# Kernel optimization log

Measured on AMD Instinct MI355X. Metric: run time of the kernel, lower is better.

The kernel has to match this reference:

```python
import jax, jax.numpy as jnp
import numpy as np

N_NODES = 100000
N_EDGES = 1600000
FEATS = 128
HIDDEN = 64
N_CLASS = 40
NEG_SLOPE = 0.01  # torch leaky_relu default


def _glorot(key, shape):
    lim = float(np.sqrt(6.0 / (shape[0] + shape[1])))
    return jax.random.uniform(key, shape, jnp.float32, -lim, lim)


def setup_inputs() -> dict:
    key = jax.random.key(0)
    ks = jax.random.split(key, 10)
    x = jax.random.normal(ks[0], (N_NODES, FEATS), jnp.float32)
    edge_index = jax.random.randint(ks[1], (2, N_EDGES), 0, N_NODES, jnp.int64)
    edge_weight = jax.random.uniform(ks[2], (N_EDGES,), jnp.float32)
    return {
        "x": x,
        "edge_index": edge_index,
        "edge_weight": edge_weight,
        "W_first": _glorot(ks[3], (FEATS, HIDDEN)),
        "b_first": jnp.zeros((HIDDEN,), jnp.float32),
        "Wc1": _glorot(ks[4], (HIDDEN, HIDDEN)),
        "bc1": jnp.zeros((HIDDEN,), jnp.float32),
        "Wc2": _glorot(ks[5], (HIDDEN, HIDDEN)),
        "bc2": jnp.zeros((HIDDEN,), jnp.float32),
        "W_out": _glorot(ks[6], (HIDDEN, N_CLASS)),
        "b_out": jnp.zeros((N_CLASS,), jnp.float32),
    }


def _gcn_norm(edge_index, edge_weight, n):
    # PyG gcn_norm with add_self_loops=True: A_hat = D^-1/2 (A + I) D^-1/2
    loop = jnp.arange(n, dtype=edge_index.dtype)
    src = jnp.concatenate([edge_index[0], loop])
    dst = jnp.concatenate([edge_index[1], loop])
    ew = jnp.concatenate([edge_weight, jnp.ones((n,), edge_weight.dtype)])
    deg = jax.ops.segment_sum(ew, dst, num_segments=n)  # degree at target
    dis = jnp.where(deg > 0, jax.lax.rsqrt(deg), 0.0)
    norm = dis[src] * ew * dis[dst]  # [E+N]
    return src, dst, norm


def _gcn_conv(h, src, dst, norm, W, b, n):
    h = h @ W                                   # [N, H]
    msg = norm[:, None] * h[src]                # gather + scale  [E+N, H]
    out = jax.ops.segment_sum(msg, dst, num_segments=n)  # scatter-add
    return out + b


def reference(x, edge_index, edge_weight, W_first, b_first, Wc1, bc1, Wc2, bc2, W_out, b_out):
    n = x.shape[0]
    src, dst, norm = _gcn_norm(edge_index, edge_weight, n)
    h = jax.nn.leaky_relu(x @ W_first + b_first, NEG_SLOPE)
    # dropout is identity in eval mode
    h = jax.nn.leaky_relu(_gcn_conv(h, src, dst, norm, Wc1, bc1, n), NEG_SLOPE)
    h = jax.nn.leaky_relu(_gcn_conv(h, src, dst, norm, Wc2, bc2, n), NEG_SLOPE)
    logits = h @ W_out + b_out
    return jax.nn.log_softmax(logits, axis=-1)
```

## Files before the change

### kernel.cpp

```cpp
#include <hip/hip_runtime.h>
#include <hip/hip_bf16.h>
#include <math.h>

#define NFEATS 128
#define NHID   64
#define NCLS   40
#define NEG_SLOPE 0.01f

#define GSH_S  9
#define GSPAN_S 512
#define GCAP_S 9216
#define SB     2048

typedef float f32x4 __attribute__((ext_vector_type(4)));
typedef int   i32x2 __attribute__((ext_vector_type(2)));

__device__ inline unsigned short f2bfu(float v) {
    union { float f; unsigned int u; } x; x.f = v;
    unsigned int r = (x.u + 0x7FFFu + ((x.u >> 16) & 1u)) >> 16;
    return (unsigned short)r;
}
__device__ inline float bf2f(unsigned short u) {
    union { unsigned int u32; float f; } x; x.u32 = ((unsigned int)u) << 16;
    return x.f;
}

__device__ inline void role_split(int i, int nA, int nB, int* ia, int* ib) {
    *ia = -1; *ib = -1;
    int m2 = 2 * min(nA, nB);
    if (i < m2) { if (i & 1) *ib = i >> 1; else *ia = i >> 1; }
    else if (nA > nB) *ia = i - nB;
    else *ib = i - nA;
}


__global__ __launch_bounds__(256) void stage_gemm1_kernel(
    const int* __restrict__ srcA, const int* __restrict__ dstA, const float* __restrict__ ew,
    int* __restrict__ gcur, int2* __restrict__ staged, int E, int nStage, int ngrp,
    const float* __restrict__ x, const float* __restrict__ W1, const float* __restrict__ b1,
    float* __restrict__ h1, int n, int nTile) {
    __shared__ __align__(16) float Ws[64 * 64];

    int ia, ib;
    role_split(blockIdx.x, nStage, nTile, &ia, &ib);
    int tid = threadIdx.x;

    if (ia >= 0) {
        int* hist = (int*)Ws;
        int* wcur = ((int*)Ws) + 256;
        if (tid < 256) hist[tid] = 0;
        __syncthreads();

        int q0 = (ia * SB) >> 2;
        int qend = min(q0 + SB / 4, E >> 2);
        int dcache[8], scache[8];
        float wcache[8];

#pragma unroll
        for (int it = 0; it < 2; ++it) {
            int q = q0 + it * 256 + tid;
            bool ok = (q < qend);
            int4 d4 = ok ? ((const int4*)dstA)[q] : make_int4(-1, -1, -1, -1);
            int4 s4 = ok ? ((const int4*)srcA)[q] : make_int4(0, 0, 0, 0);
            float4 w4 = ok ? ((const float4*)ew)[q] : make_float4(0, 0, 0, 0);
            dcache[it * 4 + 0] = d4.x; dcache[it * 4 + 1] = d4.y;
            dcache[it * 4 + 2] = d4.z; dcache[it * 4 + 3] = d4.w;
            scache[it * 4 + 0] = s4.x; scache[it * 4 + 1] = s4.y;
            scache[it * 4 + 2] = s4.z; scache[it * 4 + 3] = s4.w;
            wcache[it * 4 + 0] = w4.x; wcache[it * 4 + 1] = w4.y;
            wcache[it * 4 + 2] = w4.z; wcache[it * 4 + 3] = w4.w;
#pragma unroll
            for (int j = 0; j < 4; ++j)
                if (dcache[it * 4 + j] >= 0) atomicAdd(&hist[dcache[it * 4 + j] >> GSH_S], 1);
        }
        if (ia == nStage - 1) {
            for (int e = (E & ~3) + tid; e < E; e += 256) atomicAdd(&hist[dstA[e] >> GSH_S], 1);
        }
        __syncthreads();

        if (tid < ngrp) {
            int c = hist[tid];
            wcur[tid] = (c > 0) ? atomicAdd(&gcur[tid], c) : 0;
        }
        __syncthreads();

        int pos[8];
#pragma unroll
        for (int j = 0; j < 8; ++j) {
            int d = dcache[j];
            pos[j] = (d >= 0) ? atomicAdd(&wcur[d >> GSH_S], 1) : GCAP_S;
        }
#pragma unroll
        for (int j = 0; j < 8; ++j) {
            int d = dcache[j];
            if (d >= 0 && pos[j] < GCAP_S)
                staged[(size_t)(d >> GSH_S) * GCAP_S + pos[j]] =
                    make_int2(((d & (GSPAN_S - 1)) << 17) | scache[j], __float_as_int(wcache[j]));
        }
        if (ia == nStage - 1) {
            for (int e = (E & ~3) + tid; e < E; e += 256) {
                int d = dstA[e];
                int g = d >> GSH_S;
                int p = atomicAdd(&wcur[g], 1);
                if (p < GCAP_S)
                    staged[(size_t)g * GCAP_S + p] =
                        make_int2(((d & (GSPAN_S - 1)) << 17) | srcA[e], __float_as_int(ew[e]));
            }
        }
        return;
    }

    int c4 = (tid & 15) * 4;
    int r0 = ib * 64 + (tid >> 4) * 4;
    int rr[4];
#pragma unroll
    for (int i = 0; i < 4; ++i) rr[i] = min(r0 + i, n - 1);

    float acc[4][4] = {};
    for (int ph = 0; ph < 2; ++ph) {
        __syncthreads();
        for (int i = tid; i < 64 * 16; i += 256)
            ((float4*)Ws)[i] = ((const float4*)W1)[ph * 1024 + i];
        __syncthreads();
#pragma unroll 2
        for (int kk = 0; kk < 64; kk += 4) {
            f32x4 av[4], bv[4];
#pragma unroll
            for (int i = 0; i < 4; ++i)
                av[i] = __builtin_nontemporal_load(
                    (const f32x4*)&x[(size_t)rr[i] * NFEATS + ph * 64 + kk]);
#pragma unroll
            for (int q = 0; q < 4; ++q) bv[q] = *(const f32x4*)&Ws[(kk + q) * 64 + c4];
#pragma unroll
            for (int i = 0; i < 4; ++i) {
#pragma unroll
                for (int q = 0; q < 4; ++q) {
                    float a = av[i][q];
#pragma unroll
                    for (int j = 0; j < 4; ++j) acc[i][j] += a * bv[q][j];
                }
            }
        }
    }

#pragma unroll
    for (int i = 0; i < 4; ++i) {
        int rw = r0 + i;
        if (rw >= n) break;
        float4 o;
        float* oa = (float*)&o;
#pragma unroll
        for (int j = 0; j < 4; ++j) {
            float v = acc[i][j] + b1[c4 + j];
            oa[j] = (v > 0.0f) ? v : v * NEG_SLOPE;
        }
        *(float4*)&h1[(size_t)rw * 64 + c4] = o;
    }
}


__global__ __launch_bounds__(512) void degsort_kernel(
    const int* __restrict__ gcur, const int2* __restrict__ staged,
    int2* __restrict__ staged2, float* __restrict__ dis,
    int2* __restrict__ nodeptr, int n) {
    __shared__ float deg[GSPAN_S];
    __shared__ int hist[GSPAN_S], base[GSPAN_S], cur[GSPAN_S];

    int tid = threadIdx.x;
    int g = blockIdx.x;
    deg[tid] = 0.0f;
    hist[tid] = 0;
    __syncthreads();

    int cnt = min(gcur[g], GCAP_S);
    const int2* sl = staged + (size_t)g * GCAP_S;
    for (int i = tid; i < cnt; i += 512) {
        int2 r = sl[i];
        int dl = r.x >> 17;
        atomicAdd(&deg[dl], __int_as_float(r.y));
        atomicAdd(&hist[dl], 1);
    }
    __syncthreads();

    int node = g * GSPAN_S + tid;
    if (node < n) dis[node] = rsqrtf(1.0f + deg[tid]);

    base[tid] = hist[tid];
    __syncthreads();
    for (int off = 1; off < GSPAN_S; off <<= 1) {
        int t_ = (tid >= off) ? base[tid - off] : 0;
        __syncthreads();
        base[tid] += t_;
        __syncthreads();
    }
    int ex = base[tid] - hist[tid];
    base[tid] = ex;
    cur[tid] = ex;
    __syncthreads();

    if (node < n) nodeptr[node] = make_int2(g * GCAP_S + ex, hist[tid]);

    int2* out = staged2 + (size_t)g * GCAP_S;
    for (int i = tid; i < cnt; i += 512) {
        int2 r = sl[i];
        int dl = r.x >> 17;
        int pos = atomicAdd(&cur[dl], 1);
        out[pos] = make_int2(r.x & 0x1FFFF, r.y);
    }
}


__global__ __launch_bounds__(256) void gemm2s_kernel(
    const float* __restrict__ in, const float* __restrict__ W, const float* __restrict__ dis,
    unsigned short* __restrict__ outp, int n) {
    __shared__ __align__(16) float Ws[NHID * 64];
    int tid = threadIdx.x;
    for (int i = tid; i < NHID * 16; i += 256) ((float4*)Ws)[i] = ((const float4*)W)[i];
    __syncthreads();

    int c4 = (tid & 15) * 4;
    int r0 = blockIdx.x * 64 + (tid >> 4) * 4;
    int rr[4];
#pragma unroll
    for (int i = 0; i < 4; ++i) rr[i] = min(r0 + i, n - 1);

    float acc[4][4] = {};
#pragma unroll 2
    for (int kk = 0; kk < NHID; kk += 4) {
        f32x4 av[4], bv[4];
#pragma unroll
        for (int i = 0; i < 4; ++i)
            av[i] = __builtin_nontemporal_load((const f32x4*)&in[(size_t)rr[i] * NHID + kk]);
#pragma unroll
        for (int q = 0; q < 4; ++q) bv[q] = *(const f32x4*)&Ws[(kk + q) * 64 + c4];
#pragma unroll
        for (int i = 0; i < 4; ++i) {
#pragma unroll
            for (int q = 0; q < 4; ++q) {
                float a = av[i][q];
#pragma unroll
                for (int j = 0; j < 4; ++j) acc[i][j] += a * bv[q][j];
            }
        }
    }

#pragma unroll
    for (int i = 0; i < 4; ++i) {
        int rw = r0 + i;
        if (rw >= n) break;
        float dr = dis[rw];
        ushort4 o;
        o.x = f2bfu(dr * acc[i][0]); o.y = f2bfu(dr * acc[i][1]);
        o.z = f2bfu(dr * acc[i][2]); o.w = f2bfu(dr * acc[i][3]);
        *(ushort4*)&outp[(size_t)rw * 64 + c4] = o;
    }
}


template <int LAYER>
__global__ __launch_bounds__(256) void agg_kernel(const int2* __restrict__ nodeptr,
                                                  const int2* __restrict__ recs0,
                                                  const unsigned short* __restrict__ tb,
                                                  const float* __restrict__ dis,
                                                  const float* __restrict__ bias,
                                                  unsigned short* __restrict__ outp, int n) {
    int wv = threadIdx.x >> 6;
    int lane = threadIdx.x & 63;
    int node = blockIdx.x * 4 + wv;
    if (node >= n) return;

    int2 np = nodeptr[node];
    int start = np.x, c = np.y;
    float a0 = bf2f(tb[(size_t)node * NHID + lane]);
    float a1 = 0.0f, a2 = 0.0f, a3 = 0.0f;
    float a4 = 0.0f, a5 = 0.0f, a6 = 0.0f, a7 = 0.0f;

    const i32x2* recs = (const i32x2*)(recs0 + start);
    for (int b = 0; b < c; b += 64) {
        int rem = min(64, c - b);
        i32x2 ent = (lane < rem) ? __builtin_nontemporal_load(recs + b + lane) : (i32x2){0, 0};
        int k = 0;
        for (; k + 7 < rem; k += 8) {
            int s0 = __shfl(ent[0], k);     float w0 = __int_as_float(__shfl(ent[1], k));
            int s1 = __shfl(ent[0], k + 1); float w1 = __int_as_float(__shfl(ent[1], k + 1));
            int s2 = __shfl(ent[0], k + 2); float w2 = __int_as_float(__shfl(ent[1], k + 2));
            int s3 = __shfl(ent[0], k + 3); float w3 = __int_as_float(__shfl(ent[1], k + 3));
            int s4 = __shfl(ent[0], k + 4); float w4 = __int_as_float(__shfl(ent[1], k + 4));
            int s5 = __shfl(ent[0], k + 5); float w5 = __int_as_float(__shfl(ent[1], k + 5));
            int s6 = __shfl(ent[0], k + 6); float w6 = __int_as_float(__shfl(ent[1], k + 6));
            int s7 = __shfl(ent[0], k + 7); float w7 = __int_as_float(__shfl(ent[1], k + 7));
            a0 += w0 * bf2f(tb[(size_t)s0 * NHID + lane]);
            a1 += w1 * bf2f(tb[(size_t)s1 * NHID + lane]);
            a2 += w2 * bf2f(tb[(size_t)s2 * NHID + lane]);
            a3 += w3 * bf2f(tb[(size_t)s3 * NHID + lane]);
            a4 += w4 * bf2f(tb[(size_t)s4 * NHID + lane]);
            a5 += w5 * bf2f(tb[(size_t)s5 * NHID + lane]);
            a6 += w6 * bf2f(tb[(size_t)s6 * NHID + lane]);
            a7 += w7 * bf2f(tb[(size_t)s7 * NHID + lane]);
        }
        for (; k + 3 < rem; k += 4) {
            int s0 = __shfl(ent[0], k);     float w0 = __int_as_float(__shfl(ent[1], k));
            int s1 = __shfl(ent[0], k + 1); float w1 = __int_as_float(__shfl(ent[1], k + 1));
            int s2 = __shfl(ent[0], k + 2); float w2 = __int_as_float(__shfl(ent[1], k + 2));
            int s3 = __shfl(ent[0], k + 3); float w3 = __int_as_float(__shfl(ent[1], k + 3));
            a0 += w0 * bf2f(tb[(size_t)s0 * NHID + lane]);
            a1 += w1 * bf2f(tb[(size_t)s1 * NHID + lane]);
            a2 += w2 * bf2f(tb[(size_t)s2 * NHID + lane]);
            a3 += w3 * bf2f(tb[(size_t)s3 * NHID + lane]);
        }
        for (; k < rem; ++k) {
            int s0 = __shfl(ent[0], k); float w0 = __int_as_float(__shfl(ent[1], k));
            a0 += w0 * bf2f(tb[(size_t)s0 * NHID + lane]);
        }
    }

    float sum = ((a0 + a1) + (a2 + a3)) + ((a4 + a5) + (a6 + a7));
    float di = dis[node];
    if (LAYER == 1) {
        float h = di * sum + bias[lane];
        h = (h > 0.0f) ? h : h * NEG_SLOPE;
        outp[(size_t)node * NHID + lane] = f2bfu(di * h);
    } else {
        outp[(size_t)node * NHID + lane] = f2bfu(di * sum);
    }
}


__global__ __launch_bounds__(256) void tail_kernel(const unsigned short* __restrict__ ub,
                                                   const float* __restrict__ Wc2,
                                                   const float* __restrict__ bc2,
                                                   const float* __restrict__ Wo,
                                                   const float* __restrict__ bo,
                                                   float* __restrict__ outp, int n) {
    __shared__ __align__(16) float WsA[NHID * 64];
    __shared__ __align__(16) unsigned short hs[64 * 68];
    __shared__ float bos[NCLS];

    int tid = threadIdx.x;
    for (int i = tid; i < NHID * 16; i += 256) ((float4*)WsA)[i] = ((const float4*)Wc2)[i];
    __syncthreads();

    int c4 = (tid & 15) * 4;
    int r0l = (tid >> 4) * 4;
    int base = blockIdx.x * 64;

    int rr[4];
#pragma unroll
    for (int i = 0; i < 4; ++i) rr[i] = min(base + r0l + i, n - 1);

    float acc[4][4] = {};
#pragma unroll 2
    for (int kk = 0; kk < NHID; kk += 4) {
        f32x4 av[4], bv[4];
#pragma unroll
        for (int i = 0; i < 4; ++i) {
            ushort4 uv = *(const ushort4*)&ub[(size_t)rr[i] * NHID + kk];
            av[i][0] = bf2f(uv.x); av[i][1] = bf2f(uv.y);
            av[i][2] = bf2f(uv.z); av[i][3] = bf2f(uv.w);
        }
#pragma unroll
        for (int q = 0; q < 4; ++q) bv[q] = *(const f32x4*)&WsA[(kk + q) * 64 + c4];
#pragma unroll
        for (int i = 0; i < 4; ++i) {
#pragma unroll
            for (int q = 0; q < 4; ++q) {
                float a = av[i][q];
#pragma unroll
                for (int j = 0; j < 4; ++j) acc[i][j] += a * bv[q][j];
            }
        }
    }

#pragma unroll
    for (int i = 0; i < 4; ++i) {
#pragma unroll
        for (int j = 0; j < 4; ++j) {
            float v = acc[i][j] + bc2[c4 + j];
            v = (v > 0.0f) ? v : v * NEG_SLOPE;
            hs[(r0l + i) * 68 + c4 + j] = f2bfu(v);
        }
    }
    __syncthreads();

    for (int i = tid; i < NHID * NCLS / 4; i += 256) ((float4*)WsA)[i] = ((const float4*)Wo)[i];
    if (tid < NCLS) bos[tid] = bo[tid];
    __syncthreads();

    int row = tid >> 2;
    int c0 = (tid & 3) * 10;
    int node = base + row;

    float z[10];
#pragma unroll
    for (int j = 0; j < 10; ++j) z[j] = 0.0f;

#pragma unroll 2
    for (int k0 = 0; k0 < NHID; k0 += 4) {
        ushort4 hv = *(const ushort4*)&hs[row * 68 + k0];
        float h0 = bf2f(hv.x), h1 = bf2f(hv.y), h2 = bf2f(hv.z), h3 = bf2f(hv.w);
        const float* w0 = &WsA[(k0 + 0) * NCLS + c0];
        const float* w1 = &WsA[(k0 + 1) * NCLS + c0];
        const float* w2 = &WsA[(k0 + 2) * NCLS + c0];
        const float* w3 = &WsA[(k0 + 3) * NCLS + c0];
#pragma unroll
        for (int j = 0; j < 10; ++j)
            z[j] += h0 * w0[j] + h1 * w1[j] + h2 * w2[j] + h3 * w3[j];
    }
#pragma unroll
    for (int j = 0; j < 10; ++j) z[j] += bos[c0 + j];

    float m = z[0];
#pragma unroll
    for (int j = 1; j < 10; ++j) m = fmaxf(m, z[j]);
    m = fmaxf(m, __shfl_xor(m, 1));
    m = fmaxf(m, __shfl_xor(m, 2));

    float s = 0.0f;
#pragma unroll
    for (int j = 0; j < 10; ++j) s += expf(z[j] - m);
    s += __shfl_xor(s, 1);
    s += __shfl_xor(s, 2);
    float ls = logf(s);

    if (node < n) {
#pragma unroll
        for (int j = 0; j < 10; ++j)
            outp[(size_t)node * NCLS + c0 + j] = z[j] - m - ls;
    }
}


extern "C" void kernel_launch(void* const* d_in, const int* in_sizes, int n_in,
                              void* d_out, int out_size, void* d_ws, size_t ws_size,
                              hipStream_t stream) {
    const float* x   = (const float*)d_in[0];
    const int*   ei  = (const int*)d_in[1];
    const float* ew  = (const float*)d_in[2];
    const float* W1  = (const float*)d_in[3];
    const float* b1  = (const float*)d_in[4];
    const float* Wc1 = (const float*)d_in[5];
    const float* bc1 = (const float*)d_in[6];
    const float* Wc2 = (const float*)d_in[7];
    const float* bc2 = (const float*)d_in[8];
    const float* Wo  = (const float*)d_in[9];
    const float* bo  = (const float*)d_in[10];
    float* out = (float*)d_out;

    const int N = in_sizes[0] / NFEATS;
    const int E = in_sizes[1] / 2;
    const int* src = ei;
    const int* dst = ei + E;

    const int ngrp   = (N + GSPAN_S - 1) >> GSH_S;
    const int nStage = (E + SB - 1) / SB;
    const int nTile  = (N + 63) / 64;
    const int aggBlocks = (N + 3) / 4;

    float*          bufA  = (float*)d_ws;
    unsigned short* t1b   = (unsigned short*)(bufA + (size_t)N * NHID);
    unsigned short* h2b   = t1b + (size_t)N * NHID;
    int2*  staged  = (int2*)(h2b + (size_t)N * NHID);
    int2*  staged2 = staged + (size_t)ngrp * GCAP_S;
    float* dis     = (float*)(staged2 + (size_t)ngrp * GCAP_S);
    int*   gcur    = (int*)(dis + N);
    int2*  nodeptr = (int2*)(gcur + ((ngrp + 1) & ~1));

    hipMemsetAsync(gcur, 0, ngrp * sizeof(int), stream);

    stage_gemm1_kernel<<<nStage + nTile, 256, 0, stream>>>(
        src, dst, ew, gcur, staged, E, nStage, ngrp, x, W1, b1, bufA, N, nTile);

    degsort_kernel<<<ngrp, 512, 0, stream>>>(gcur, staged, staged2, dis, nodeptr, N);

    gemm2s_kernel<<<nTile, 256, 0, stream>>>(bufA, Wc1, dis, t1b, N);

    agg_kernel<1><<<aggBlocks, 256, 0, stream>>>(nodeptr, staged2, t1b, dis, bc1, h2b, N);

    agg_kernel<2><<<aggBlocks, 256, 0, stream>>>(nodeptr, staged2, h2b, dis, nullptr, t1b, N);

    tail_kernel<<<nTile, 256, 0, stream>>>(t1b, Wc2, bc2, Wo, bo, out, N);
}
```

Baseline: 264.8 us.

## Fold symmetric normalization into edge weights and vectorize aggregation gathers

Splits degree computation from sorting so the sort pass can precompute the full normalized edge weight dis[src]*w*dis[dst]. It runs the sort concurrently with the second GEMM in one launch via role splitting. The GEMM no longer scales rows by dis, and the aggregation kernel no longer rescales its output. The aggregation kernel now uses 16-lane groups, each handling a different edge with 8-byte bf16x4 loads, then reduces across groups with xor shuffles. The goal is fewer gather instructions per edge and less per-node scaling, at the cost of an extra small launch and a cross-lane reduction.

```diff
diff --git a/kernel.cpp b/kernel.cpp
--- a/kernel.cpp
+++ b/kernel.cpp
@@ -23,6 +23,12 @@
 __device__ inline float bf2f(unsigned short u) {
     union { unsigned int u32; float f; } x; x.u32 = ((unsigned int)u) << 16;
     return x.f;
+}
+__device__ inline float bflo(unsigned int u) {
+    union { unsigned int v; float f; } x; x.v = u << 16; return x.f;
+}
+__device__ inline float bfhi(unsigned int u) {
+    union { unsigned int v; float f; } x; x.v = u & 0xFFFF0000u; return x.f;
 }
 
 __device__ inline void role_split(int i, int nA, int nB, int* ia, int* ib) {
@@ -159,67 +165,83 @@
 }
 
 
-__global__ __launch_bounds__(512) void degsort_kernel(
-    const int* __restrict__ gcur, const int2* __restrict__ staged,
-    int2* __restrict__ staged2, float* __restrict__ dis,
-    int2* __restrict__ nodeptr, int n) {
+__global__ __launch_bounds__(512) void deg_dis_kernel(const int* __restrict__ gcur,
+                                                      const int2* __restrict__ staged,
+                                                      float* __restrict__ dis, int n) {
     __shared__ float deg[GSPAN_S];
-    __shared__ int hist[GSPAN_S], base[GSPAN_S], cur[GSPAN_S];
-
     int tid = threadIdx.x;
     int g = blockIdx.x;
     deg[tid] = 0.0f;
-    hist[tid] = 0;
     __syncthreads();
 
     int cnt = min(gcur[g], GCAP_S);
-    const int2* sl = staged + (size_t)g * GCAP_S;
+    const i32x2* sl = (const i32x2*)(staged + (size_t)g * GCAP_S);
     for (int i = tid; i < cnt; i += 512) {
-        int2 r = sl[i];
-        int dl = r.x >> 17;
-        atomicAdd(&deg[dl], __int_as_float(r.y));
-        atomicAdd(&hist[dl], 1);
+        i32x2 r = sl[i];
+        atomicAdd(&deg[r[0] >> 17], __int_as_float(r[1]));
     }
     __syncthreads();
 
     int node = g * GSPAN_S + tid;
     if (node < n) dis[node] = rsqrtf(1.0f + deg[tid]);
-
-    base[tid] = hist[tid];
+}
+
+
+__global__ __launch_bounds__(512) void sort_gemm2_kernel(
+    const int* __restrict__ gcur, const int2* __restrict__ staged,
+    int2* __restrict__ staged2, const float* __restrict__ dis,
+    int2* __restrict__ nodeptr, int ngrp,
+    const float* __restrict__ in, const float* __restrict__ W,
+    unsigned short* __restrict__ outp, int n, int nTile2) {
+    __shared__ __align__(16) float Ws[NHID * 64];
+    __shared__ int hist[GSPAN_S], base[GSPAN_S], cur[GSPAN_S];
+    __shared__ float disl[GSPAN_S];
+
+    int ia, ib;
+    role_split(blockIdx.x, ngrp, nTile2, &ia, &ib);
+    int tid = threadIdx.x;
+
+    if (ia >= 0) {
+        int g = ia;
+        int cnt = min(gcur[g], GCAP_S);
+        const int2* sl = staged + (size_t)g * GCAP_S;
+        hist[tid] = 0;
+        int node = g * GSPAN_S + tid;
+        disl[tid] = (node < n) ? dis[node] : 0.0f;
+        __syncthreads();
+        for (int i = tid; i < cnt; i += 512) atomicAdd(&hist[sl[i].x >> 17], 1);
+        __syncthreads();
+        base[tid] = hist[tid];
+        __syncthreads();
+        for (int off = 1; off < GSPAN_S; off <<= 1) {
+            int t_ = (tid >= off) ? base[tid - off] : 0;
+            __syncthreads();
+            base[tid] += t_;
+            __syncthreads();
+        }
+        int ex = base[tid] - hist[tid];
+        cur[tid] = ex;
+        if (node < n) nodeptr[node] = make_int2(g * GCAP_S + ex, hist[tid]);
+        __syncthreads();
+        int2* out = staged2 + (size_t)g * GCAP_S;
+        for (int i = tid; i < cnt; i += 512) {
+            int2 r = sl[i];
+            int dl = r.x >> 17, s = r.x & 0x1FFFF;
+            float w = dis[s] * __int_as_float(r.y) * disl[dl];
+            int pos = atomicAdd(&cur[dl], 1);
+            out[pos] = make_int2(s, __float_as_int(w));
+        }
+        return;
+    }
+
+    for (int i = tid; i < NHID * 16; i += 512) ((float4*)Ws)[i] = ((const float4*)W)[i];
     __syncthreads();
-    for (int off = 1; off < GSPAN_S; off <<= 1) {
-        int t_ = (tid >= off) ? base[tid - off] : 0;
-        __syncthreads();
-        base[tid] += t_;
-        __syncthreads();
-    }
-    int ex = base[tid] - hist[tid];
-    base[tid] = ex;
-    cur[tid] = ex;
-    __syncthreads();
-
-    if (node < n) nodeptr[node] = make_int2(g * GCAP_S + ex, hist[tid]);
-
-    int2* out = staged2 + (size_t)g * GCAP_S;
-    for (int i = tid; i < cnt; i += 512) {
-        int2 r = sl[i];
-        int dl = r.x >> 17;
-        int pos = atomicAdd(&cur[dl], 1);
-        out[pos] = make_int2(r.x & 0x1FFFF, r.y);
-    }
-}
-
-
-__global__ __launch_bounds__(256) void gemm2s_kernel(
-    const float* __restrict__ in, const float* __restrict__ W, const float* __restrict__ dis,
-    unsigned short* __restrict__ outp, int n) {
-    __shared__ __align__(16) float Ws[NHID * 64];
-    int tid = threadIdx.x;
-    for (int i = tid; i < NHID * 16; i += 256) ((float4*)Ws)[i] = ((const float4*)W)[i];
-    __syncthreads();
-
-    int c4 = (tid & 15) * 4;
-    int r0 = blockIdx.x * 64 + (tid >> 4) * 4;
+
+    int half = tid >> 8;
+    int t2 = tid & 255;
+    int tile = ib * 2 + half;
+    int c4 = (t2 & 15) * 4;
+    int r0 = tile * 64 + (t2 >> 4) * 4;
     int rr[4];
 #pragma unroll
     for (int i = 0; i < 4; ++i) rr[i] = min(r0 + i, n - 1);
@@ -248,10 +270,9 @@
     for (int i = 0; i < 4; ++i) {
         int rw = r0 + i;
         if (rw >= n) break;
-        float dr = dis[rw];
         ushort4 o;
-        o.x = f2bfu(dr * acc[i][0]); o.y = f2bfu(dr * acc[i][1]);
-        o.z = f2bfu(dr * acc[i][2]); o.w = f2bfu(dr * acc[i][3]);
+        o.x = f2bfu(acc[i][0]); o.y = f2bfu(acc[i][1]);
+        o.z = f2bfu(acc[i][2]); o.w = f2bfu(acc[i][3]);
         *(ushort4*)&outp[(size_t)rw * 64 + c4] = o;
     }
 }
@@ -271,57 +292,66 @@
 
     int2 np = nodeptr[node];
     int start = np.x, c = np.y;
-    float a0 = bf2f(tb[(size_t)node * NHID + lane]);
-    float a1 = 0.0f, a2 = 0.0f, a3 = 0.0f;
-    float a4 = 0.0f, a5 = 0.0f, a6 = 0.0f, a7 = 0.0f;
+    int grp = lane >> 4;
+    int r16 = lane & 15;
+    float di = dis[node];
+
+    f32x4 a0 = {0, 0, 0, 0}, a1 = {0, 0, 0, 0}, a2 = {0, 0, 0, 0}, a3 = {0, 0, 0, 0};
+
+    if (grp == 0) {
+        uint2 uv = *(const uint2*)&tb[(size_t)node * NHID + r16 * 4];
+        float d2 = di * di;
+        a0[0] += d2 * bflo(uv.x); a0[1] += d2 * bfhi(uv.x);
+        a0[2] += d2 * bflo(uv.y); a0[3] += d2 * bfhi(uv.y);
+    }
 
     const i32x2* recs = (const i32x2*)(recs0 + start);
     for (int b = 0; b < c; b += 64) {
         int rem = min(64, c - b);
-        i32x2 ent = (lane < rem) ? __builtin_nontemporal_load(recs + b + lane) : (i32x2){0, 0};
-        int k = 0;
-        for (; k + 7 < rem; k += 8) {
-            int s0 = __shfl(ent[0], k);     float w0 = __int_as_float(__shfl(ent[1], k));
-            int s1 = __shfl(ent[0], k + 1); float w1 = __int_as_float(__shfl(ent[1], k + 1));
-            int s2 = __shfl(ent[0], k + 2); float w2 = __int_as_float(__shfl(ent[1], k + 2));
-            int s3 = __shfl(ent[0], k + 3); float w3 = __int_as_float(__shfl(ent[1], k + 3));
-            int s4 = __shfl(ent[0], k + 4); float w4 = __int_as_float(__shfl(ent[1], k + 4));
-            int s5 = __shfl(ent[0], k + 5); float w5 = __int_as_float(__shfl(ent[1], k + 5));
-            int s6 = __shfl(ent[0], k + 6); float w6 = __int_as_float(__shfl(ent[1], k + 6));
-            int s7 = __shfl(ent[0], k + 7); float w7 = __int_as_float(__shfl(ent[1], k + 7));
-            a0 += w0 * bf2f(tb[(size_t)s0 * NHID + lane]);
-            a1 += w1 * bf2f(tb[(size_t)s1 * NHID + lane]);
-            a2 += w2 * bf2f(tb[(size_t)s2 * NHID + lane]);
-            a3 += w3 * bf2f(tb[(size_t)s3 * NHID + lane]);
-            a4 += w4 * bf2f(tb[(size_t)s4 * NHID + lane]);
-            a5 += w5 * bf2f(tb[(size_t)s5 * NHID + lane]);
-            a6 += w6 * bf2f(tb[(size_t)s6 * NHID + lane]);
-            a7 += w7 * bf2f(tb[(size_t)s7 * NHID + lane]);
-        }
-        for (; k + 3 < rem; k += 4) {
-            int s0 = __shfl(ent[0], k);     float w0 = __int_as_float(__shfl(ent[1], k));
-            int s1 = __shfl(ent[0], k + 1); float w1 = __int_as_float(__shfl(ent[1], k + 1));
-            int s2 = __shfl(ent[0], k + 2); float w2 = __int_as_float(__shfl(ent[1], k + 2));
-            int s3 = __shfl(ent[0], k + 3); float w3 = __int_as_float(__shfl(ent[1], k + 3));
-            a0 += w0 * bf2f(tb[(size_t)s0 * NHID + lane]);
-            a1 += w1 * bf2f(tb[(size_t)s1 * NHID + lane]);
-            a2 += w2 * bf2f(tb[(size_t)s2 * NHID + lane]);
-            a3 += w3 * bf2f(tb[(size_t)s3 * NHID + lane]);
-        }
-        for (; k < rem; ++k) {
-            int s0 = __shfl(ent[0], k); float w0 = __int_as_float(__shfl(ent[1], k));
-            a0 += w0 * bf2f(tb[(size_t)s0 * NHID + lane]);
-        }
-    }
-
-    float sum = ((a0 + a1) + (a2 + a3)) + ((a4 + a5) + (a6 + a7));
-    float di = dis[node];
-    if (LAYER == 1) {
-        float h = di * sum + bias[lane];
-        h = (h > 0.0f) ? h : h * NEG_SLOPE;
-        outp[(size_t)node * NHID + lane] = f2bfu(di * h);
-    } else {
-        outp[(size_t)node * NHID + lane] = f2bfu(di * sum);
+        i32x2 ent = (lane < rem) ? recs[b + lane] : (i32x2){0, 0};
+        for (int k = 0; k < rem; k += 16) {
+            int e0 = k + grp, e1 = k + 4 + grp, e2 = k + 8 + grp, e3 = k + 12 + grp;
+            int s0 = __shfl(ent[0], e0); float w0 = __int_as_float(__shfl(ent[1], e0));
+            int s1 = __shfl(ent[0], e1); float w1 = __int_as_float(__shfl(ent[1], e1));
+            int s2 = __shfl(ent[0], e2); float w2 = __int_as_float(__shfl(ent[1], e2));
+            int s3 = __shfl(ent[0], e3); float w3 = __int_as_float(__shfl(ent[1], e3));
+            uint2 u0 = *(const uint2*)&tb[(size_t)s0 * NHID + r16 * 4];
+            uint2 u1 = *(const uint2*)&tb[(size_t)s1 * NHID + r16 * 4];
+            uint2 u2 = *(const uint2*)&tb[(size_t)s2 * NHID + r16 * 4];
+            uint2 u3 = *(const uint2*)&tb[(size_t)s3 * NHID + r16 * 4];
+            a0[0] += w0 * bflo(u0.x); a0[1] += w0 * bfhi(u0.x);
+            a0[2] += w0 * bflo(u0.y); a0[3] += w0 * bfhi(u0.y);
+            a1[0] += w1 * bflo(u1.x); a1[1] += w1 * bfhi(u1.x);
+            a1[2] += w1 * bflo(u1.y); a1[3] += w1 * bfhi(u1.y);
+            a2[0] += w2 * bflo(u2.x); a2[1] += w2 * bfhi(u2.x);
+            a2[2] += w2 * bflo(u2.y); a2[3] += w2 * bfhi(u2.y);
+            a3[0] += w3 * bflo(u3.x); a3[1] += w3 * bfhi(u3.x);
+            a3[2] += w3 * bflo(u3.y); a3[3] += w3 * bfhi(u3.y);
+        }
+    }
+
+    f32x4 acc;
+#pragma unroll
+    for (int j = 0; j < 4; ++j) acc[j] = (a0[j] + a1[j]) + (a2[j] + a3[j]);
+#pragma unroll
+    for (int j = 0; j < 4; ++j) {
+        acc[j] += __shfl_xor(acc[j], 16);
+        acc[j] += __shfl_xor(acc[j], 32);
+    }
+
+    if (lane < 16) {
+        ushort4 o;
+        unsigned short* op = (unsigned short*)&o;
+#pragma unroll
+        for (int j = 0; j < 4; ++j) {
+            float v = acc[j];
+            if (LAYER == 1) {
+                v += bias[r16 * 4 + j];
+                v = (v > 0.0f) ? v : v * NEG_SLOPE;
+            }
+            op[j] = f2bfu(v);
+        }
+        *(ushort4*)&outp[(size_t)node * NHID + r16 * 4] = o;
     }
 }
 
@@ -454,6 +484,7 @@
     const int ngrp   = (N + GSPAN_S - 1) >> GSH_S;
     const int nStage = (E + SB - 1) / SB;
     const int nTile  = (N + 63) / 64;
+    const int nTile2 = (N + 127) / 128;
     const int aggBlocks = (N + 3) / 4;
 
     float*          bufA  = (float*)d_ws;
@@ -470,9 +501,10 @@
     stage_gemm1_kernel<<<nStage + nTile, 256, 0, stream>>>(
         src, dst, ew, gcur, staged, E, nStage, ngrp, x, W1, b1, bufA, N, nTile);
 
-    degsort_kernel<<<ngrp, 512, 0, stream>>>(gcur, staged, staged2, dis, nodeptr, N);
-
-    gemm2s_kernel<<<nTile, 256, 0, stream>>>(bufA, Wc1, dis, t1b, N);
+    deg_dis_kernel<<<ngrp, 512, 0, stream>>>(gcur, staged, dis, N);
+
+    sort_gemm2_kernel<<<ngrp + nTile2, 512, 0, stream>>>(
+        gcur, staged, staged2, dis, nodeptr, ngrp, bufA, Wc1, t1b, N, nTile2);
 
     agg_kernel<1><<<aggBlocks, 256, 0, stream>>>(nodeptr, staged2, t1b, dis, bc1, h2b, N);
 
```

Result: slower. 271.1 us (+2.4%).
